# Performance work log

Measured on AMD Instinct MI355X. Metric: run time of the kernel, lower is better.

The kernel has to match this reference:

```python
import jax, jax.numpy as jnp
import numpy as np

jax.config.update("jax_enable_x64", True)  # torch uses int64 labels with wrapping arithmetic

N = 100_000   # nodes
E = 3_200_000 # edges
D = 128       # label classes (argmax dim)
NUM_ITERATIONS = 3


def setup_inputs() -> dict:
    key = jax.random.key(0)
    k1, k2 = jax.random.split(key)
    x = jax.random.normal(k1, (N, D), dtype=jnp.float32)
    edge_index = jax.random.randint(k2, (2, E), 0, N, dtype=jnp.int64)
    return {"x": x, "edge_index": edge_index}


def _edge_exponents(row):
    """For each edge e, number of edges AFTER e (in edge order) sharing the same row.

    The torch loop computes neighborhood[r] = neighborhood[r]*31 + labels[c]
    sequentially over edges, i.e. for a row-group with targets c_1..c_k (edge order)
    the result is sum_j labels[c_j] * 31**(k - j). The exponent (k - j) is exactly
    the count of later same-row edges.
    """
    e = row.shape[0]
    order = jnp.argsort(row, stable=True)          # stable sort preserves edge order within groups
    srow = row[order]
    first = jnp.searchsorted(srow, srow, side="left")   # group start index
    last = jnp.searchsorted(srow, srow, side="right")   # group end index (exclusive)
    pos = jnp.arange(e) - first                          # position within group
    exp_sorted = (last - first) - 1 - pos                # edges remaining after this one
    return jnp.zeros(e, dtype=jnp.int64).at[order].set(exp_sorted)


def reference(x, edge_index):
    labels = jnp.argmax(x, axis=-1).astype(jnp.int64) if x.ndim > 1 else x.astype(jnp.int64)
    row, col = edge_index[0], edge_index[1]
    exps = _edge_exponents(row)
    # 31**exp in wrapping int64 arithmetic; exponentiation-by-squaring mod 2^64
    # matches the sequential multiply-add mod 2^64 of the torch loop.
    pow31 = jnp.power(jnp.int64(31), exps)
    history = [labels]
    for _ in range(NUM_ITERATIONS):
        vals = labels[col] * pow31                       # [E] per-edge weighted labels
        labels = jax.ops.segment_sum(vals, row, num_segments=N)  # ordered hash accumulate
        history.append(labels)
    return (labels, *history)
```

## Files before the change

kernel.cpp:

```cpp
#include <hip/hip_runtime.h>
#include <hip/hip_bf16.h>


#define WL_D 128
#define NCH 1024
#define GRID_F 2048
#define BT 512
#define MSDW 8
#define BBITS 8
#define BROWS 256
#define NBK 512
#define RLSHIFT 23
#define COLMASK ((1u << RLSHIFT) - 1u)
#define CMAX 10240
#define NBMAX 7

template <int BITS>
__device__ inline unsigned long long match_key(unsigned v) {
    unsigned long long m = ~0ull;
    #pragma unroll
    for (int b = 0; b < BITS; ++b) {
        unsigned long long s = __ballot((v >> b) & 1u);
        m &= ((v >> b) & 1u) ? s : ~s;
    }
    return m;
}

__global__ void __launch_bounds__(BT)
k_hist_argmax(const float* __restrict__ x, const int* __restrict__ ei,
              unsigned* __restrict__ lab0, unsigned* __restrict__ hist,
              int N, int E, int chunk, int nbuckets) {
    __shared__ unsigned h[NBK];
    int b = blockIdx.x, t = threadIdx.x, lane = t & 63, w = t >> 6;
    if (b < NCH) {
        for (int i = t; i < nbuckets; i += BT) h[i] = 0u;
        __syncthreads();
        int base = b * chunk, lim = min(base + chunk, E);
        for (int e = base + t; e < lim; e += BT)
            atomicAdd(&h[((unsigned)ei[e]) >> BBITS], 1u);
        __syncthreads();
        for (int v = t; v < nbuckets; v += BT) hist[(size_t)v * NCH + b] = h[v];
    }
    for (int r = b * MSDW + w; r < N; r += GRID_F * MSDW) {
        const float2* xr = (const float2*)(x + (size_t)r * WL_D);
        float2 v = xr[lane];
        float bv; int bi;
        if (v.y > v.x) { bv = v.y; bi = 2 * lane + 1; } else { bv = v.x; bi = 2 * lane; }
        #pragma unroll
        for (int off = 32; off > 0; off >>= 1) {
            float ov = __shfl_down(bv, off, 64);
            int   oi = __shfl_down(bi, off, 64);
            if (ov > bv || (ov == bv && oi < bi)) { bv = ov; bi = oi; }
        }
        if (lane == 0) lab0[r] = (unsigned)bi;
    }
}

__global__ void __launch_bounds__(BT)
k_scan_tile(unsigned* __restrict__ hist, unsigned* __restrict__ bsums, int L) {
    __shared__ unsigned smem[BT];
    int b = blockIdx.x, t = threadIdx.x;
    int i0 = b * 1024;
    unsigned v0 = (i0 + 2 * t     < L) ? hist[i0 + 2 * t]     : 0u;
    unsigned v1 = (i0 + 2 * t + 1 < L) ? hist[i0 + 2 * t + 1] : 0u;
    unsigned s = v0 + v1;
    smem[t] = s;
    __syncthreads();
    for (int o = 1; o < BT; o <<= 1) {
        unsigned u = (t >= o) ? smem[t - o] : 0u;
        __syncthreads();
        smem[t] += u;
        __syncthreads();
    }
    unsigned excl = smem[t] - s;
    if (i0 + 2 * t     < L) hist[i0 + 2 * t]     = excl;
    if (i0 + 2 * t + 1 < L) hist[i0 + 2 * t + 1] = excl + v0;
    if (t == BT - 1) bsums[b] = smem[BT - 1];
}

__global__ void __launch_bounds__(BT)
k_scan_sums(unsigned* __restrict__ bsums, int ntiles) {
    __shared__ unsigned smem[BT];
    int t = threadIdx.x;
    unsigned v = (t < ntiles) ? bsums[t] : 0u;
    smem[t] = v;
    __syncthreads();
    for (int o = 1; o < BT; o <<= 1) {
        unsigned u = (t >= o) ? smem[t - o] : 0u;
        __syncthreads();
        smem[t] += u;
        __syncthreads();
    }
    if (t < ntiles) bsums[t] = smem[t] - v;
}

__global__ void __launch_bounds__(BT)
k_transp(const unsigned* __restrict__ hist, const unsigned* __restrict__ bsums,
         unsigned* __restrict__ histT, int nbuckets) {
    __shared__ unsigned tl[64][65];
    int vtiles = (nbuckets + 63) / 64;
    int bx = blockIdx.x % vtiles;
    int by = blockIdx.x / vtiles;
    int tx = threadIdx.x & 63, ty = threadIdx.x >> 6;
    int v0 = bx * 64, b0 = by * 64;
    #pragma unroll
    for (int r = 0; r < 8; ++r) {
        int row = r * 8 + ty;
        int v = v0 + row;
        size_t idx = (size_t)v * NCH + (b0 + tx);
        tl[row][tx] = (v < nbuckets) ? (hist[idx] + bsums[idx >> 10]) : 0u;
    }
    __syncthreads();
    #pragma unroll
    for (int r = 0; r < 8; ++r) {
        int row = r * 8 + ty;
        int v = v0 + tx;
        if (v < nbuckets) histT[(size_t)(b0 + row) * nbuckets + v] = tl[tx][row];
    }
}

__global__ void __launch_bounds__(BT)
k_scatter(const int* __restrict__ ei, const unsigned* __restrict__ histT,
          unsigned* __restrict__ buf, int E, int chunk, int nbuckets) {
    __shared__ unsigned wbase[MSDW * NBK];
    int b = blockIdx.x, t = threadIdx.x, lane = t & 63, w = t >> 6;
    unsigned long long lmask = (1ull << lane) - 1ull;
    for (int i = t; i < MSDW * NBK; i += BT) wbase[i] = 0u;
    __syncthreads();
    int base = b * chunk, lim = min(base + chunk, E);
    int sub  = (chunk + MSDW - 1) / MSDW;
    int wbeg = base + w * sub;
    int wend = min(wbeg + sub, lim);
    int nbat = (wbeg < wend) ? ((wend - wbeg + 63) >> 6) : 0;
    unsigned r_[NBMAX];
    #pragma unroll
    for (int k = 0; k < NBMAX; ++k) {
        int e = wbeg + k * 64 + lane;
        r_[k] = (e < wend) ? (unsigned)ei[e] : 0u;
    }
    #pragma unroll
    for (int k = 0; k < NBMAX; ++k) {
        if (k >= nbat) break;
        int e = wbeg + k * 64 + lane;
        bool act = (e < wend);
        unsigned v = act ? (r_[k] >> BBITS) : (NBK - 1u);
        unsigned long long m = match_key<9>(v);
        unsigned before = (unsigned)__popcll(m & lmask);
        unsigned total  = (unsigned)__popcll(m);
        if (act && before == 0u) wbase[w * NBK + v] += total;
    }
    for (int k = NBMAX; k < nbat; ++k) {
        int e = wbeg + k * 64 + lane;
        bool act = (e < wend);
        unsigned v = act ? (((unsigned)ei[e]) >> BBITS) : (NBK - 1u);
        unsigned long long m = match_key<9>(v);
        unsigned before = (unsigned)__popcll(m & lmask);
        unsigned total  = (unsigned)__popcll(m);
        if (act && before == 0u) wbase[w * NBK + v] += total;
    }
    __syncthreads();
    for (int v = t; v < nbuckets; v += BT) {
        unsigned g = histT[(size_t)b * nbuckets + v];
        #pragma unroll
        for (int w2 = 0; w2 < MSDW; ++w2) {
            unsigned cnt = wbase[w2 * NBK + v];
            wbase[w2 * NBK + v] = g;
            g += cnt;
        }
    }
    __syncthreads();
    unsigned c_[NBMAX];
    #pragma unroll
    for (int k = 0; k < NBMAX; ++k) {
        int e = wbeg + k * 64 + lane;
        c_[k] = (e < wend) ? (unsigned)ei[(size_t)E + e] : 0u;
    }
    #pragma unroll
    for (int k = 0; k < NBMAX; ++k) {
        if (k >= nbat) break;
        int e = wbeg + k * 64 + lane;
        bool act = (e < wend);
        unsigned r = r_[k], col = c_[k];
        unsigned v = act ? (r >> BBITS) : (NBK - 1u);
        unsigned long long m = match_key<9>(v);
        unsigned before = (unsigned)__popcll(m & lmask);
        unsigned total  = (unsigned)__popcll(m);
        int leader = __ffsll(m) - 1;
        unsigned base0 = 0;
        if (act && before == 0u) { base0 = wbase[w * NBK + v]; wbase[w * NBK + v] = base0 + total; }
        base0 = __shfl(base0, leader, 64);
        if (act) buf[base0 + before] = ((r & (BROWS - 1u)) << RLSHIFT) | col;
    }
    for (int k = NBMAX; k < nbat; ++k) {
        int e = wbeg + k * 64 + lane;
        bool act = (e < wend);
        unsigned r   = act ? (unsigned)ei[e] : 0u;
        unsigned col = act ? (unsigned)ei[(size_t)E + e] : 0u;
        unsigned v = act ? (r >> BBITS) : (NBK - 1u);
        unsigned long long m = match_key<9>(v);
        unsigned before = (unsigned)__popcll(m & lmask);
        unsigned total  = (unsigned)__popcll(m);
        int leader = __ffsll(m) - 1;
        unsigned base0 = 0;
        if (act && before == 0u) { base0 = wbase[w * NBK + v]; wbase[w * NBK + v] = base0 + total; }
        base0 = __shfl(base0, leader, 64);
        if (act) buf[base0 + before] = ((r & (BROWS - 1u)) << RLSHIFT) | col;
    }
}

__global__ void __launch_bounds__(BT)
k_bucket(const unsigned* __restrict__ buf, const unsigned* __restrict__ hist,
         const unsigned* __restrict__ bsums, unsigned* __restrict__ csr,
         unsigned* __restrict__ rs_g, int N, int E, int nbuckets) {
    __shared__ unsigned data2[CMAX];
    __shared__ unsigned h2[MSDW * BROWS];
    __shared__ unsigned offs[BROWS];
    int bb = blockIdx.x, t = threadIdx.x, lane = t & 63, w = t >> 6;
    unsigned long long lmask = (1ull << lane) - 1ull;
    size_t i0 = (size_t)bb * NCH;
    unsigned start = hist[i0] + bsums[i0 >> 10];
    unsigned end;
    if (bb + 1 < nbuckets) { size_t i1 = (size_t)(bb + 1) * NCH; end = hist[i1] + bsums[i1 >> 10]; }
    else end = (unsigned)E;
    unsigned len = end - start;
    bool lds_ok = (len <= CMAX);
    for (int i = t; i < MSDW * BROWS; i += BT) h2[i] = 0u;
    __syncthreads();
    unsigned sub  = (len + MSDW - 1u) / MSDW;
    unsigned wbeg = w * sub;
    unsigned wend = min(wbeg + sub, len);
    int nbat = (wbeg < wend) ? (int)((wend - wbeg + 63u) >> 6) : 0;
    for (int bt2 = 0; bt2 < nbat; ++bt2) {
        unsigned i = wbeg + (unsigned)(bt2 * 64 + lane);
        bool act = (i < wend);
        unsigned v = act ? (buf[start + i] >> RLSHIFT) : 511u;
        unsigned long long m = match_key<9>(v);
        unsigned before = (unsigned)__popcll(m & lmask);
        unsigned total  = (unsigned)__popcll(m);
        if (act && before == 0u) h2[w * BROWS + v] += total;
    }
    __syncthreads();
    unsigned hv = 0;
    if (t < BROWS) {
        #pragma unroll
        for (int w2 = 0; w2 < MSDW; ++w2) hv += h2[w2 * BROWS + t];
        offs[t] = hv;
    }
    __syncthreads();
    for (int o = 1; o < BROWS; o <<= 1) {
        unsigned s = (t < BROWS && t >= o) ? offs[t - o] : 0u;
        __syncthreads();
        if (t < BROWS) offs[t] += s;
        __syncthreads();
    }
    if (t < BROWS) {
        unsigned excl = offs[t] - hv;
        int row = bb * BROWS + t;
        if (row < N) rs_g[row] = start + excl;
        unsigned g = lds_ok ? excl : (start + excl);
        #pragma unroll
        for (int w2 = 0; w2 < MSDW; ++w2) {
            unsigned cnt = h2[w2 * BROWS + t];
            h2[w2 * BROWS + t] = g;
            g += cnt;
        }
    }
    __syncthreads();
    for (int bt2 = 0; bt2 < nbat; ++bt2) {
        unsigned i = wbeg + (unsigned)(bt2 * 64 + lane);
        bool act = (i < wend);
        unsigned p = act ? buf[start + i] : 0u;
        unsigned v = act ? (p >> RLSHIFT) : 511u;
        unsigned long long m = match_key<9>(v);
        unsigned before = (unsigned)__popcll(m & lmask);
        unsigned total  = (unsigned)__popcll(m);
        int leader = __ffsll(m) - 1;
        unsigned base0 = 0;
        if (act && before == 0u) { base0 = h2[w * BROWS + v]; h2[w * BROWS + v] = base0 + total; }
        base0 = __shfl(base0, leader, 64);
        if (act) {
            if (lds_ok) data2[base0 + before] = p & COLMASK;
            else        csr[base0 + before]   = p & COLMASK;
        }
    }
    __syncthreads();
    if (lds_ok) for (unsigned i = t; i < len; i += BT) csr[start + i] = data2[i];
}

__global__ void __launch_bounds__(BT)
k_prop(const unsigned* __restrict__ csr, const unsigned* __restrict__ rs,
       const unsigned* __restrict__ lin, unsigned* __restrict__ lout,
       int N, int E) {
    int g = (blockIdx.x * BT + threadIdx.x) >> 2;
    int l = threadIdx.x & 3;
    if (g >= N) return;
    unsigned s = rs[g];
    unsigned e = (g + 1 < N) ? rs[g + 1] : (unsigned)E;
    unsigned d = e - s;
    unsigned h = 0u;
    unsigned M = (d > (unsigned)l) ? ((d - (unsigned)l + 3u) >> 2) : 0u;
    for (unsigned m = 0; m < M; ++m) {
        unsigned col = csr[s + (unsigned)l + 4u * m];
        h = h * 923521u + lin[col];
    }
    if (M) {
        unsigned T = d - 1u - (unsigned)l - 4u * (M - 1u);
        unsigned p = ((T & 1u) ? 31u : 1u) * ((T & 2u) ? 961u : 1u);
        h *= p;
    }
    h += __shfl_xor(h, 1, 64);
    h += __shfl_xor(h, 2, 64);
    if (l == 0) lout[g] = h;
}

__global__ void __launch_bounds__(BT)
k_out(const unsigned* __restrict__ l0, const unsigned* __restrict__ l1,
      const unsigned* __restrict__ l2, const unsigned* __restrict__ l3,
      int* __restrict__ out, int N) {
    for (int i = blockIdx.x * BT + threadIdx.x; i < N; i += 256 * BT) {
        int a0 = (int)l0[i], a1 = (int)l1[i], a2 = (int)l2[i], a3 = (int)l3[i];
        out[i]         = a3;
        out[N + i]     = a0;
        out[2 * N + i] = a1;
        out[3 * N + i] = a2;
        out[4 * N + i] = a3;
    }
}

extern "C" void kernel_launch(void* const* d_in, const int* in_sizes, int n_in,
                              void* d_out, int out_size, void* d_ws, size_t ws_size,
                              hipStream_t stream) {
    const float* x  = (const float*)d_in[0];
    const int*   ei = (const int*)d_in[1];
    int* out = (int*)d_out;

    int N = in_sizes[0] / WL_D;
    int E = in_sizes[1] / 2;
    int chunk    = (E + NCH - 1) / NCH;
    int nbuckets = (N + BROWS - 1) / BROWS;
    int L        = nbuckets * NCH;
    int ntiles   = (L + 1023) / 1024;
    int vtiles   = (nbuckets + 63) / 64;
    int btiles   = NCH / 64;
    int pgrid    = (4 * N + BT - 1) / BT;

    unsigned* ws   = (unsigned*)d_ws;
    unsigned* lab0 = ws;
    unsigned* lab1 = lab0 + N;
    unsigned* lab2 = lab1 + N;
    unsigned* lab3 = lab2 + N;
    unsigned* rs   = lab3 + N;
    unsigned* bs   = rs + N;
    unsigned* hist = bs + 1024;
    unsigned* buf  = hist + L;
    unsigned* csr  = buf + E;
    unsigned* histT = csr;

    k_hist_argmax<<<GRID_F, BT, 0, stream>>>(x, ei, lab0, hist, N, E, chunk, nbuckets);
    k_scan_tile<<<ntiles, BT, 0, stream>>>(hist, bs, L);
    k_scan_sums<<<1, BT, 0, stream>>>(bs, ntiles);
    k_transp<<<vtiles * btiles, BT, 0, stream>>>(hist, bs, histT, nbuckets);
    k_scatter<<<NCH, BT, 0, stream>>>(ei, histT, buf, E, chunk, nbuckets);
    k_bucket<<<nbuckets, BT, 0, stream>>>(buf, hist, bs, csr, rs, N, E, nbuckets);
    k_prop<<<pgrid, BT, 0, stream>>>(csr, rs, lab0, lab1, N, E);
    k_prop<<<pgrid, BT, 0, stream>>>(csr, rs, lab1, lab2, N, E);
    k_prop<<<pgrid, BT, 0, stream>>>(csr, rs, lab2, lab3, N, E);
    k_out<<<256, BT, 0, stream>>>(lab0, lab1, lab2, lab3, out, N);
}
```

Before: 238.7 us.

## Widen propagation to 8 lanes per row, fuse output copy, halve histogram chunks

Propagation now splits each row across 8 lanes, with a 31^8 stride multiplier and a three-step shuffle reduction, which exposes more memory-level parallelism for the gathers. The last propagation pass is fused with the output write, removing the separate output kernel and one label buffer. The argmax pass handles two rows per wavefront using float4 loads, and the histogram chunk count drops from 1024 to 512, with NBMAX raised to match. Fewer chunks shrink the scan and transpose work but make each chunk larger, which may put more load on the scatter and bucket kernels.

```diff
diff --git a/kernel.cpp b/kernel.cpp
--- a/kernel.cpp
+++ b/kernel.cpp
@@ -3,7 +3,7 @@
 
 
 #define WL_D 128
-#define NCH 1024
+#define NCH 512
 #define GRID_F 2048
 #define BT 512
 #define MSDW 8
@@ -13,7 +13,8 @@
 #define RLSHIFT 23
 #define COLMASK ((1u << RLSHIFT) - 1u)
 #define CMAX 10240
-#define NBMAX 7
+#define NBMAX 13
+#define HP8 2487512833u
 
 template <int BITS>
 __device__ inline unsigned long long match_key(unsigned v) {
@@ -41,18 +42,24 @@
         __syncthreads();
         for (int v = t; v < nbuckets; v += BT) hist[(size_t)v * NCH + b] = h[v];
     }
-    for (int r = b * MSDW + w; r < N; r += GRID_F * MSDW) {
-        const float2* xr = (const float2*)(x + (size_t)r * WL_D);
-        float2 v = xr[lane];
-        float bv; int bi;
-        if (v.y > v.x) { bv = v.y; bi = 2 * lane + 1; } else { bv = v.x; bi = 2 * lane; }
+    int half = lane >> 5, li = lane & 31;
+    for (int pr = b * MSDW + w; 2 * pr < N; pr += GRID_F * MSDW) {
+        int r = 2 * pr + half;
+        float bv = -3.4e38f; int bi = 0;
+        if (r < N) {
+            float4 v = ((const float4*)(x + (size_t)r * WL_D))[li];
+            bv = v.x; bi = 4 * li;
+            if (v.y > bv) { bv = v.y; bi = 4 * li + 1; }
+            if (v.z > bv) { bv = v.z; bi = 4 * li + 2; }
+            if (v.w > bv) { bv = v.w; bi = 4 * li + 3; }
+        }
         #pragma unroll
-        for (int off = 32; off > 0; off >>= 1) {
-            float ov = __shfl_down(bv, off, 64);
-            int   oi = __shfl_down(bi, off, 64);
+        for (int off = 16; off > 0; off >>= 1) {
+            float ov = __shfl_down(bv, off, 32);
+            int   oi = __shfl_down(bi, off, 32);
             if (ov > bv || (ov == bv && oi < bi)) { bv = ov; bi = oi; }
         }
-        if (lane == 0) lab0[r] = (unsigned)bi;
+        if (li == 0 && r < N) lab0[r] = (unsigned)bi;
     }
 }
 
@@ -287,43 +294,57 @@
     if (lds_ok) for (unsigned i = t; i < len; i += BT) csr[start + i] = data2[i];
 }
 
-__global__ void __launch_bounds__(BT)
-k_prop(const unsigned* __restrict__ csr, const unsigned* __restrict__ rs,
-       const unsigned* __restrict__ lin, unsigned* __restrict__ lout,
-       int N, int E) {
-    int g = (blockIdx.x * BT + threadIdx.x) >> 2;
-    int l = threadIdx.x & 3;
-    if (g >= N) return;
+__device__ inline unsigned horner8(const unsigned* __restrict__ csr,
+                                   const unsigned* __restrict__ rs,
+                                   const unsigned* __restrict__ lin,
+                                   int g, int l, int N, int E) {
     unsigned s = rs[g];
     unsigned e = (g + 1 < N) ? rs[g + 1] : (unsigned)E;
     unsigned d = e - s;
     unsigned h = 0u;
-    unsigned M = (d > (unsigned)l) ? ((d - (unsigned)l + 3u) >> 2) : 0u;
+    unsigned M = (d > (unsigned)l) ? ((d - (unsigned)l + 7u) >> 3) : 0u;
     for (unsigned m = 0; m < M; ++m) {
-        unsigned col = csr[s + (unsigned)l + 4u * m];
-        h = h * 923521u + lin[col];
+        unsigned col = csr[s + (unsigned)l + 8u * m];
+        h = h * HP8 + lin[col];
     }
     if (M) {
-        unsigned T = d - 1u - (unsigned)l - 4u * (M - 1u);
-        unsigned p = ((T & 1u) ? 31u : 1u) * ((T & 2u) ? 961u : 1u);
+        unsigned T = d - 1u - (unsigned)l - 8u * (M - 1u);
+        unsigned p = ((T & 1u) ? 31u : 1u) * ((T & 2u) ? 961u : 1u)
+                   * ((T & 4u) ? 923521u : 1u);
         h *= p;
     }
     h += __shfl_xor(h, 1, 64);
     h += __shfl_xor(h, 2, 64);
+    h += __shfl_xor(h, 4, 64);
+    return h;
+}
+
+__global__ void __launch_bounds__(BT)
+k_prop(const unsigned* __restrict__ csr, const unsigned* __restrict__ rs,
+       const unsigned* __restrict__ lin, unsigned* __restrict__ lout,
+       int N, int E) {
+    int idx = blockIdx.x * BT + threadIdx.x;
+    int g = idx >> 3, l = idx & 7;
+    if (g >= N) return;
+    unsigned h = horner8(csr, rs, lin, g, l, N, E);
     if (l == 0) lout[g] = h;
 }
 
 __global__ void __launch_bounds__(BT)
-k_out(const unsigned* __restrict__ l0, const unsigned* __restrict__ l1,
-      const unsigned* __restrict__ l2, const unsigned* __restrict__ l3,
-      int* __restrict__ out, int N) {
-    for (int i = blockIdx.x * BT + threadIdx.x; i < N; i += 256 * BT) {
-        int a0 = (int)l0[i], a1 = (int)l1[i], a2 = (int)l2[i], a3 = (int)l3[i];
-        out[i]         = a3;
-        out[N + i]     = a0;
-        out[2 * N + i] = a1;
-        out[3 * N + i] = a2;
-        out[4 * N + i] = a3;
+k_prop_final(const unsigned* __restrict__ csr, const unsigned* __restrict__ rs,
+             const unsigned* __restrict__ lin, const unsigned* __restrict__ l0,
+             const unsigned* __restrict__ l1, int* __restrict__ out,
+             int N, int E, int pgrid) {
+    int idx = blockIdx.x * BT + threadIdx.x;
+    int g = idx >> 3, l = idx & 7;
+    if (g < N) {
+        unsigned h = horner8(csr, rs, lin, g, l, N, E);
+        if (l == 0) { out[g] = (int)h; out[4 * N + g] = (int)h; }
+    }
+    for (int i = idx; i < N; i += pgrid * BT) {
+        out[N + i]     = (int)l0[i];
+        out[2 * N + i] = (int)l1[i];
+        out[3 * N + i] = (int)lin[i];
     }
 }
 
@@ -342,14 +363,13 @@
     int ntiles   = (L + 1023) / 1024;
     int vtiles   = (nbuckets + 63) / 64;
     int btiles   = NCH / 64;
-    int pgrid    = (4 * N + BT - 1) / BT;
+    int pgrid    = (8 * N + BT - 1) / BT;
 
     unsigned* ws   = (unsigned*)d_ws;
     unsigned* lab0 = ws;
     unsigned* lab1 = lab0 + N;
     unsigned* lab2 = lab1 + N;
-    unsigned* lab3 = lab2 + N;
-    unsigned* rs   = lab3 + N;
+    unsigned* rs   = lab2 + N;
     unsigned* bs   = rs + N;
     unsigned* hist = bs + 1024;
     unsigned* buf  = hist + L;
@@ -364,6 +384,5 @@
     k_bucket<<<nbuckets, BT, 0, stream>>>(buf, hist, bs, csr, rs, N, E, nbuckets);
     k_prop<<<pgrid, BT, 0, stream>>>(csr, rs, lab0, lab1, N, E);
     k_prop<<<pgrid, BT, 0, stream>>>(csr, rs, lab1, lab2, N, E);
-    k_prop<<<pgrid, BT, 0, stream>>>(csr, rs, lab2, lab3, N, E);
-    k_out<<<256, BT, 0, stream>>>(lab0, lab1, lab2, lab3, out, N);
-}
+    k_prop_final<<<pgrid, BT, 0, stream>>>(csr, rs, lab2, lab0, lab1, out, N, E, pgrid);
+}
```

Result: faster. 216.6 us (-9.2%).
